# Performance work log

Hardware: AMD Instinct MI355X
Metric: run time of the kernel (lower is better)

## Reference

```python
import jax, jax.numpy as jnp
import numpy as np

DIM = 512      # model dim
HEADS = 8      # num heads
DH = 64        # dim_head (hard-coded in PerformerBlock)
M = 266        # nb_features = int(DH * ln(DH)) per performer_pytorch default
EPS = 1e-4     # softmax_kernel eps


def _gaussian_orthogonal_matrix(rng, m, d):
    # Faithful to performer_pytorch gaussian_orthogonal_random_matrix (scaling=0):
    # stacked QR-orthogonalized dxd blocks, rows rescaled by chi-distributed norms.
    blocks = []
    for _ in range(m // d + 1):
        q, _ = np.linalg.qr(rng.standard_normal((d, d)))
        blocks.append(q.T)
    mat = np.concatenate(blocks, 0)[:m]
    mult = np.linalg.norm(rng.standard_normal((m, d)), axis=1)
    return (mult[:, None] * mat).astype(np.float32)


def setup_inputs() -> dict:
    key = jax.random.key(0)
    ks = jax.random.split(key, 6)
    inner = HEADS * DH
    s = 0.02
    x = jax.random.normal(ks[0], (4, 4096, DIM), dtype=jnp.float32)
    Wq = jax.random.normal(ks[1], (inner, DIM), dtype=jnp.float32) * s
    Wk = jax.random.normal(ks[2], (inner, DIM), dtype=jnp.float32) * s
    Wv = jax.random.normal(ks[3], (inner, DIM), dtype=jnp.float32) * s
    Wo = jax.random.normal(ks[4], (DIM, inner), dtype=jnp.float32) * s
    bo = jnp.zeros((DIM,), dtype=jnp.float32)
    proj = jnp.asarray(_gaussian_orthogonal_matrix(np.random.default_rng(0), M, DH))
    return {"x": x, "Wq": Wq, "Wk": Wk, "Wv": Wv, "Wo": Wo, "bo": bo, "proj": proj}


def _softmax_kernel(t, proj, is_query):
    # t: (b,h,n,DH), proj: (M,DH)
    normalizer = DH ** -0.25          # 1/sqrt(sqrt(d))
    ratio = M ** -0.5
    td = jnp.einsum('bhnd,md->bhnm', t * normalizer, proj)
    diag = jnp.sum(t * t, axis=-1, keepdims=True) * 0.5 * (normalizer ** 2)
    if is_query:
        mx = jax.lax.stop_gradient(jnp.max(td, axis=-1, keepdims=True))
    else:
        mx = jax.lax.stop_gradient(jnp.max(td, axis=(-1, -2), keepdims=True))
    return ratio * (jnp.exp(td - diag - mx) + EPS)


def reference(x, Wq, Wk, Wv, Wo, bo, proj):
    b, n, _ = x.shape
    def heads(w):
        return jnp.einsum('bnd,ed->bne', x, w).reshape(b, n, HEADS, DH).transpose(0, 2, 1, 3)
    q, k, v = heads(Wq), heads(Wk), heads(Wv)  # (b,h,n,DH)
    qp = _softmax_kernel(q, proj, True)        # (b,h,n,M)
    kp = _softmax_kernel(k, proj, False)       # (b,h,n,M)
    # non-causal linear attention
    k_sum = jnp.sum(kp, axis=-2)                               # (b,h,M)
    d_inv = 1.0 / jnp.einsum('bhnm,bhm->bhn', qp, k_sum)       # (b,h,n)
    context = jnp.einsum('bhnm,bhnd->bhmd', kp, v)             # (b,h,M,DH)
    out = jnp.einsum('bhmd,bhnm,bhn->bhnd', context, qp, d_inv)
    out = out.transpose(0, 2, 1, 3).reshape(b, n, HEADS * DH)
    attn_out = out @ Wo.T + bo
    return x + attn_out
```

## Files before the change

### kernel.cpp

```cpp
#include <hip/hip_runtime.h>

#define N_ 4096
#define DIM_ 512
#define H_ 8
#define DH_ 64
#define M_ 266
#define MP_ 272
#define MP2_ 288
#define MP3_ 320
#define SLABM_ 280
#define NZ_ 8
#define NT_ 16384
#define BH_ 32

#define NORMC 0.3535533905932738f
#define RATIOC 0.06131393394849658f
#define EPSK 1e-4f
#define DIAGC 0.0625f
#define KA 0.51006971f
#define LOG2R -4.0276408f
#define LOG2E 1.4426950408889634f
#define REPS 6.131393e-6f

#define PROJP_B 0ul
#define KMAX_B  40960ul
#define KSUMA_B 41088ul
#define WO_B    82048ul
#define CTXT_B  606336ul
#define DIAGQ_B 1785984ul
#define DIAGK_B 2048128ul
#define XBF_B   2310272ul
#define WQ_B    19087488ul
#define WK_B    19611776ul
#define WV_B    20136064ul
#define CTXA_B  2310272ul
#define Q_B     20660352ul
#define K_B     37437568ul
#define VT_B    54214784ul
#define RMAXQ_B 70992000ul

typedef __bf16 bf16x8 __attribute__((ext_vector_type(8)));
typedef float f32x4 __attribute__((ext_vector_type(4)));
#define MFMA16(a, b, c) __builtin_amdgcn_mfma_f32_16x16x32_bf16((a), (b), (c), 0, 0, 0)

typedef __attribute__((address_space(1))) const unsigned int* gas_t;
typedef __attribute__((address_space(3))) unsigned int* las_t;
__device__ __forceinline__ void gload16(const void* g, void* l) {
  __builtin_amdgcn_global_load_lds((gas_t)g, (las_t)l, 16, 0, 0);
}

__device__ __forceinline__ float bfu(unsigned short u) {
  union { unsigned int i; float f; } x; x.i = ((unsigned int)u) << 16; return x.f;
}
__device__ __forceinline__ unsigned short f2bf(float f) {
  union { float f; unsigned int i; } u; u.f = f;
  unsigned int r = u.i + 0x7fffu + ((u.i >> 16) & 1u);
  return (unsigned short)(r >> 16);
}
__device__ __forceinline__ void atomicMaxF(float* addr, float val) {
  int* ai = (int*)addr;
  while (true) {
    float cur = __int_as_float(*(volatile int*)ai);
    if (val <= cur) break;
    int old = atomicCAS(ai, __float_as_int(cur), __float_as_int(val));
    if (old == __float_as_int(cur)) break;
  }
}

__global__ void cvt_kernel(const float* __restrict__ src, unsigned short* __restrict__ dst, int n) {
  int i = (blockIdx.x * 256 + threadIdx.x) * 4;
  const int stride = gridDim.x * 1024;
  for (; i < n; i += stride) {
    const float4 v = *(const float4*)(src + i);
    ushort4 u;
    u.x = f2bf(v.x); u.y = f2bf(v.y); u.z = f2bf(v.z); u.w = f2bf(v.w);
    *(ushort4*)(dst + i) = u;
  }
}

__global__ void setup_kernel(const float* __restrict__ proj,
                             unsigned short* __restrict__ projp,
                             float* __restrict__ kmax,
                             float* __restrict__ ksuma) {
  const int i = blockIdx.x * 256 + threadIdx.x;
  const int stride = gridDim.x * 256;
  for (int j = i; j < MP3_ * DH_; j += stride)
    projp[j] = (j < M_ * DH_) ? f2bf(proj[j]) : (unsigned short)0;
  for (int j = i; j < BH_; j += stride) kmax[j] = -3e38f;
  for (int j = i; j < BH_ * MP3_; j += stride) ksuma[j] = 0.f;
}

__global__ __launch_bounds__(256) void qkv_mfma(
    const unsigned short* __restrict__ x, const unsigned short* __restrict__ Wq,
    const unsigned short* __restrict__ Wk, const unsigned short* __restrict__ Wv,
    unsigned short* __restrict__ Q, unsigned short* __restrict__ K,
    unsigned short* __restrict__ VT) {
  __shared__ unsigned short As[128 * 64];
  __shared__ unsigned short Bs[128 * 64];
  const int z = blockIdx.z;
  const unsigned short* W = (z == 0) ? Wq : (z == 1) ? Wk : Wv;
  const int t0 = blockIdx.x * 128, e0 = blockIdx.y * 128;
  const int tid = threadIdx.x;
  const int wv = tid >> 6, lane = tid & 63;
  const int r = lane & 15, q = lane >> 4;
  const int wr = (wv >> 1) * 64, wc = (wv & 1) * 64;
  f32x4 acc[4][4];
#pragma unroll
  for (int i = 0; i < 4; ++i)
#pragma unroll
    for (int j = 0; j < 4; ++j) acc[i][j] = (f32x4){0.f, 0.f, 0.f, 0.f};
  const int lrow = lane >> 3, lcol = (lane & 7) * 8;
  for (int k0 = 0; k0 < DIM_; k0 += 64) {
#pragma unroll
    for (int j = 0; j < 4; ++j) {
      const int rr = wv * 32 + j * 8;
      gload16(&x[(size_t)(t0 + rr + lrow) * DIM_ + k0 + lcol], &As[rr * 64]);
      gload16(&W[(size_t)(e0 + rr + lrow) * DIM_ + k0 + lcol], &Bs[rr * 64]);
    }
    __syncthreads();
#pragma unroll
    for (int kc = 0; kc < 2; ++kc) {
      bf16x8 af[4], bfr[4];
#pragma unroll
      for (int rt = 0; rt < 4; ++rt)
        af[rt] = *(const bf16x8*)&As[(wr + rt * 16 + r) * 64 + kc * 32 + q * 8];
#pragma unroll
      for (int ct = 0; ct < 4; ++ct)
        bfr[ct] = *(const bf16x8*)&Bs[(wc + ct * 16 + r) * 64 + kc * 32 + q * 8];
#pragma unroll
      for (int rt = 0; rt < 4; ++rt)
#pragma unroll
        for (int ct = 0; ct < 4; ++ct)
          acc[rt][ct] = MFMA16(af[rt], bfr[ct], acc[rt][ct]);
    }
    __syncthreads();
  }
  if (z < 2) {
    unsigned short* dst = (z == 0) ? Q : K;
#pragma unroll
    for (int rt = 0; rt < 4; ++rt) {
#pragma unroll
      for (int ct = 0; ct < 4; ++ct) {
        const int e = e0 + wc + ct * 16 + r;
#pragma unroll
        for (int i = 0; i < 4; ++i) {
          const int t = t0 + wr + rt * 16 + q * 4 + i;
          dst[(size_t)t * DIM_ + e] = f2bf(acc[rt][ct][i]);
        }
      }
    }
  } else {
#pragma unroll
    for (int rt = 0; rt < 4; ++rt) {
      const int t = t0 + wr + rt * 16 + q * 4;
      const int b_ = t >> 12, n = t & (N_ - 1);
#pragma unroll
      for (int ct = 0; ct < 4; ++ct) {
        const int e = e0 + wc + ct * 16 + r;
        const int h = e >> 6, dh = e & 63;
        ushort4 pk;
        pk.x = f2bf(acc[rt][ct][0]); pk.y = f2bf(acc[rt][ct][1]);
        pk.z = f2bf(acc[rt][ct][2]); pk.w = f2bf(acc[rt][ct][3]);
        *(ushort4*)&VT[((size_t)((b_ * H_ + h) * DH_ + dh)) * N_ + n] = pk;
      }
    }
  }
}

__global__ void diag_kernel(const unsigned short* __restrict__ Q,
                            const unsigned short* __restrict__ K,
                            unsigned short* __restrict__ dq, unsigned short* __restrict__ dk) {
  const int i = blockIdx.x * 256 + threadIdx.x;
  const int bh = i >> 12, n = i & (N_ - 1);
  const int b_ = bh >> 3, h = bh & 7;
  const unsigned short* src = ((blockIdx.y == 0) ? Q : K) + (size_t)(b_ * N_ + n) * DIM_ + h * DH_;
  float s = 0.f;
#pragma unroll
  for (int c = 0; c < 16; ++c) {
    const ushort4 u = ((const ushort4*)src)[c];
    const float a = bfu(u.x), b2 = bfu(u.y), cc = bfu(u.z), d = bfu(u.w);
    s += a * a + b2 * b2 + cc * cc + d * d;
  }
  ((blockIdx.y == 0) ? dq : dk)[i] = f2bf(s * DIAGC);
}

__global__ __launch_bounds__(256) void kmax_mfma(
    const unsigned short* __restrict__ K, const unsigned short* __restrict__ Qb,
    const unsigned short* __restrict__ projp,
    float* __restrict__ kmax, float* __restrict__ rmaxq) {
  __shared__ unsigned short sP[MP_][72];
  __shared__ float wm[4];
  const int bh = blockIdx.x, n0 = blockIdx.y * 256;
  const int tid = threadIdx.x;
  const int wv = tid >> 6, lane = tid & 63;
  const int r = lane & 15, q = lane >> 4;
  const int b_ = bh >> 3, h = bh & 7;
  for (int c = tid; c < MP_ * 4; c += 256) {
    const int row = c >> 2, cb = (c & 3) * 8;
    *(uint4*)&sP[row][cb] = *(const uint4*)&projp[row * DH_ + cb];
  }
  bf16x8 kb[4][2], qb[4][2];
  const int nbase = n0 + wv * 64;
#pragma unroll
  for (int st = 0; st < 4; ++st) {
    const size_t off = (size_t)(b_ * N_ + nbase + st * 16 + r) * DIM_ + h * DH_;
    kb[st][0] = *(const bf16x8*)(K + off + q * 8);
    kb[st][1] = *(const bf16x8*)(K + off + 32 + q * 8);
    qb[st][0] = *(const bf16x8*)(Qb + off + q * 8);
    qb[st][1] = *(const bf16x8*)(Qb + off + 32 + q * 8);
  }
  __syncthreads();
  float km = -3e38f;
  float qm[4] = {-3e38f, -3e38f, -3e38f, -3e38f};
  for (int mt = 0; mt < 17; ++mt) {
    const bf16x8 p0 = *(const bf16x8*)&sP[mt * 16 + r][q * 8];
    const bf16x8 p1 = *(const bf16x8*)&sP[mt * 16 + r][32 + q * 8];
#pragma unroll
    for (int st = 0; st < 4; ++st) {
      f32x4 ka = (f32x4){0.f, 0.f, 0.f, 0.f};
      ka = MFMA16(p0, kb[st][0], ka);
      ka = MFMA16(p1, kb[st][1], ka);
      f32x4 qa = (f32x4){0.f, 0.f, 0.f, 0.f};
      qa = MFMA16(p0, qb[st][0], qa);
      qa = MFMA16(p1, qb[st][1], qa);
#pragma unroll
      for (int i = 0; i < 4; ++i) {
        const int m = mt * 16 + q * 4 + i;
        if (m < M_) {
          km = fmaxf(km, ka[i]);
          qm[st] = fmaxf(qm[st], qa[i]);
        }
      }
    }
  }
#pragma unroll
  for (int st = 0; st < 4; ++st) {
    float v = qm[st];
    v = fmaxf(v, __shfl_xor(v, 16, 64));
    v = fmaxf(v, __shfl_xor(v, 32, 64));
    if (q == 0) rmaxq[bh * N_ + nbase + st * 16 + r] = v;
  }
  for (int s2 = 1; s2 < 64; s2 <<= 1) km = fmaxf(km, __shfl_xor(km, s2, 64));
  if (lane == 0) wm[wv] = km;
  __syncthreads();
  if (tid == 0) {
    const float m = fmaxf(fmaxf(wm[0], wm[1]), fmaxf(wm[2], wm[3])) * NORMC;
    atomicMaxF(&kmax[bh], m);
  }
}

__global__ __launch_bounds__(256) void ctxfused_mfma(
    const unsigned short* __restrict__ K, const unsigned short* __restrict__ VT,
    const unsigned short* __restrict__ projp, const unsigned short* __restrict__ diag_k,
    const float* __restrict__ kmaxv, float* __restrict__ ksuma,
    float* __restrict__ slab) {
  __shared__ unsigned short kll[64][72];
  __shared__ unsigned short vtl[64][72];
  __shared__ unsigned short kpl[64][72];
  __shared__ float dgl[64];
  const int bh = blockIdx.x, m0 = blockIdx.y * 64, zi = blockIdx.z;
  const int nbase = zi * 512;
  const int tid = threadIdx.x;
  const int wv = tid >> 6, lane = tid & 63;
  const int r = lane & 15, q = lane >> 4;
  const int b_ = bh >> 3, h = bh & 7;
  const float km = kmaxv[bh];
  const unsigned short* prow = projp + (size_t)(m0 + wv * 16 + r) * DH_;
  const bf16x8 p0 = *(const bf16x8*)(prow + q * 8);
  const bf16x8 p1 = *(const bf16x8*)(prow + 32 + q * 8);
  const unsigned short* kbase = K + (size_t)(b_ * N_) * DIM_ + h * DH_;
  const unsigned short* vbase = VT + (size_t)bh * DH_ * N_;
  f32x4 cacc[4];
#pragma unroll
  for (int i = 0; i < 4; ++i) cacc[i] = (f32x4){0.f, 0.f, 0.f, 0.f};
  float ksa[4] = {0.f, 0.f, 0.f, 0.f};
  for (int nc = 0; nc < 8; ++nc) {
    const int n0c = nbase + nc * 64;
#pragma unroll
    for (int j = 0; j < 4; ++j) {
      const int idx = tid + j * 256;
      const int rr = idx >> 4, c4 = (idx & 15) << 2;
      *(ushort4*)&kll[rr][c4] = *(const ushort4*)&kbase[(size_t)(n0c + rr) * DIM_ + c4];
      *(ushort4*)&vtl[rr][c4] = *(const ushort4*)&vbase[(size_t)rr * N_ + n0c + c4];
    }
    if (tid < 16) {
      const ushort4 du = *(const ushort4*)&diag_k[bh * N_ + n0c + tid * 4];
      dgl[tid * 4 + 0] = bfu(du.x); dgl[tid * 4 + 1] = bfu(du.y);
      dgl[tid * 4 + 2] = bfu(du.z); dgl[tid * 4 + 3] = bfu(du.w);
    }
    __syncthreads();
#pragma unroll
    for (int nt = 0; nt < 4; ++nt) {
      const bf16x8 kb0 = *(const bf16x8*)&kll[nt * 16 + r][q * 8];
      const bf16x8 kb1 = *(const bf16x8*)&kll[nt * 16 + r][32 + q * 8];
      f32x4 acc = (f32x4){0.f, 0.f, 0.f, 0.f};
      acc = MFMA16(p0, kb0, acc);
      acc = MFMA16(p1, kb1, acc);
      const float dgk = dgl[nt * 16 + r];
#pragma unroll
      for (int i = 0; i < 4; ++i) {
        const int m = m0 + wv * 16 + q * 4 + i;
        float kp = 0.f;
        if (m < M_) {
          const float arg = fminf(NORMC * acc[i] - dgk - km, 0.f);
          kp = RATIOC * (__expf(arg) + EPSK);
        }
        kpl[wv * 16 + q * 4 + i][nt * 16 + r] = f2bf(kp);
        ksa[i] += kp;
      }
    }
    __syncthreads();
    {
      const bf16x8 a0 = *(const bf16x8*)&kpl[wv * 16 + r][q * 8];
      const bf16x8 a1 = *(const bf16x8*)&kpl[wv * 16 + r][32 + q * 8];
#pragma unroll
      for (int ct = 0; ct < 4; ++ct) {
        const bf16x8 b0 = *(const bf16x8*)&vtl[ct * 16 + r][q * 8];
        const bf16x8 b1 = *(const bf16x8*)&vtl[ct * 16 + r][32 + q * 8];
        cacc[ct] = MFMA16(a0, b0, cacc[ct]);
        cacc[ct] = MFMA16(a1, b1, cacc[ct]);
      }
    }
    __syncthreads();
  }
#pragma unroll
  for (int i = 0; i < 4; ++i)
    for (int s2 = 1; s2 < 16; s2 <<= 1) ksa[i] += __shfl_xor(ksa[i], s2, 64);
  if (r == 0) {
#pragma unroll
    for (int i = 0; i < 4; ++i)
      atomicAdd(&ksuma[bh * MP3_ + m0 + wv * 16 + q * 4 + i], ksa[i]);
  }
  float* sl = slab + (size_t)(bh * NZ_ + zi) * SLABM_ * DH_;
#pragma unroll
  for (int ct = 0; ct < 4; ++ct) {
#pragma unroll
    for (int i = 0; i < 4; ++i) {
      const int m = m0 + wv * 16 + q * 4 + i;
      if (m < SLABM_) sl[(size_t)m * DH_ + ct * 16 + r] = cacc[ct][i];
    }
  }
}

__global__ __launch_bounds__(256) void pack_kernel(const float* __restrict__ slab,
                                                   unsigned short* __restrict__ ctxT) {
  __shared__ float t[64][65];
  const int bh = blockIdx.x, m0 = blockIdx.y * 64;
  const int tid = threadIdx.x;
  const int mr = tid >> 4, d4 = (tid & 15) * 4;
#pragma unroll
  for (int pass = 0; pass < 4; ++pass) {
    const int ml = pass * 16 + mr;
    const int m = m0 + ml;
    float4 s = {0.f, 0.f, 0.f, 0.f};
    if (m < SLABM_) {
#pragma unroll
      for (int z = 0; z < NZ_; ++z) {
        const float4 v =
            *(const float4*)&slab[((size_t)(bh * NZ_ + z) * SLABM_ + m) * DH_ + d4];
        s.x += v.x; s.y += v.y; s.z += v.z; s.w += v.w;
      }
    }
    t[ml][d4 + 0] = s.x; t[ml][d4 + 1] = s.y; t[ml][d4 + 2] = s.z; t[ml][d4 + 3] = s.w;
  }
  __syncthreads();
  const int mc = tid & 63, dbase = tid >> 6;
  const int mo = m0 + mc;
  if (mo < MP2_) {
#pragma unroll
    for (int j = 0; j < 16; ++j) {
      const int d = dbase + j * 4;
      ctxT[((size_t)bh * DH_ + d) * MP2_ + mo] = f2bf(t[mc][d]);
    }
  }
}

__global__ __launch_bounds__(256) void qpout_mfma(
    const unsigned short* __restrict__ Qb, const unsigned short* __restrict__ projp,
    const float* __restrict__ rmaxq,
    const unsigned short* __restrict__ diag_q, const float* __restrict__ ksuma,
    const unsigned short* __restrict__ ctxT, unsigned short* __restrict__ attn) {
  __shared__ union SM {
    unsigned short sP[MP_][72];
    unsigned int qps[4][16][149];
  } sm;
  const int bh = blockIdx.x, n0 = blockIdx.y * 64;
  const int tid = threadIdx.x;
  const int wv = tid >> 6, lane = tid & 63;
  const int r = lane & 15, q = lane >> 4;
  const int b_ = bh >> 3, h = bh & 7;
  for (int c = tid; c < MP_ * 4; c += 256) {
    const int row = c >> 2, cb = (c & 3) * 8;
    *(uint4*)&sm.sP[row][cb] = *(const uint4*)&projp[row * DH_ + cb];
  }
  bf16x8 qb0, qb1;
  {
    const unsigned short* qrow = Qb + (size_t)(b_ * N_ + n0 + wv * 16 + r) * DIM_ + h * DH_;
    qb0 = *(const bf16x8*)(qrow + q * 8);
    qb1 = *(const bf16x8*)(qrow + 32 + q * 8);
  }
  const float rm = rmaxq[bh * N_ + n0 + wv * 16 + r];
  const float dg = bfu(diag_q[bh * N_ + n0 + wv * 16 + r]);
  const float Cl = LOG2R - dg * LOG2E - rm * KA;
  __syncthreads();
  unsigned int pk0[17], pk1[17];
  float part = 0.f;
#pragma unroll
  for (int mt = 0; mt < 17; ++mt) {
    const bf16x8 p0 = *(const bf16x8*)&sm.sP[mt * 16 + r][q * 8];
    const bf16x8 p1 = *(const bf16x8*)&sm.sP[mt * 16 + r][32 + q * 8];
    f32x4 acc = (f32x4){0.f, 0.f, 0.f, 0.f};
    acc = MFMA16(p0, qb0, acc);
    acc = MFMA16(p1, qb1, acc);
    const f32x4 kl = *(const f32x4*)&ksuma[bh * MP3_ + mt * 16 + q * 4];
    {
      const float s0 = fminf(acc[0] * KA + Cl, LOG2R);
      const float s1 = fminf(acc[1] * KA + Cl, LOG2R);
      const float e0 = exp2f(s0) + REPS;
      const float e1 = exp2f(s1) + REPS;
      unsigned int pkk;
      asm("v_cvt_pk_bf16_f32 %0, %1, %2" : "=v"(pkk) : "v"(e0), "v"(e1));
      pk0[mt] = pkk;
      union { unsigned int u; float f; } lo, hi;
      lo.u = pkk << 16; hi.u = pkk & 0xffff0000u;
      part += lo.f * kl[0] + hi.f * kl[1];
    }
    {
      const float s0 = fminf(acc[2] * KA + Cl, LOG2R);
      const float s1 = fminf(acc[3] * KA + Cl, LOG2R);
      const float e0 = exp2f(s0) + REPS;
      const float e1 = exp2f(s1) + REPS;
      unsigned int pkk;
      asm("v_cvt_pk_bf16_f32 %0, %1, %2" : "=v"(pkk) : "v"(e0), "v"(e1));
      pk1[mt] = pkk;
      union { unsigned int u; float f; } lo, hi;
      lo.u = pkk << 16; hi.u = pkk & 0xffff0000u;
      part += lo.f * kl[2] + hi.f * kl[3];
    }
  }
  __syncthreads();
#pragma unroll
  for (int mt = 0; mt < 17; ++mt)
    *(uint2*)&sm.qps[wv][r][mt * 8 + q * 2] = make_uint2(pk0[mt], pk1[mt]);
  *(uint2*)&sm.qps[wv][r][136 + q * 2] = make_uint2(0u, 0u);
  part += __shfl_xor(part, 16, 64);
  part += __shfl_xor(part, 32, 64);
  const float dinv = 1.f / fmaxf(part, 1e-30f);
  f32x4 oacc[4];
#pragma unroll
  for (int i = 0; i < 4; ++i) oacc[i] = (f32x4){0.f, 0.f, 0.f, 0.f};
  const unsigned short* cbase = ctxT + (size_t)bh * DH_ * MP2_;
#pragma unroll
  for (int kc = 0; kc < 9; ++kc) {
    const bf16x8 af = *(const bf16x8*)&sm.qps[wv][r][kc * 16 + q * 4];
#pragma unroll
    for (int dt = 0; dt < 4; ++dt) {
      const bf16x8 bfr = *(const bf16x8*)&cbase[(size_t)(dt * 16 + r) * MP2_ + kc * 32 + q * 8];
      oacc[dt] = MFMA16(af, bfr, oacc[dt]);
    }
  }
  float dv[4];
#pragma unroll
  for (int i = 0; i < 4; ++i)
    dv[i] = __shfl(dinv, (lane & 48) | (q * 4 + i), 64);
#pragma unroll
  for (int dt = 0; dt < 4; ++dt) {
    const int d = dt * 16 + r;
#pragma unroll
    for (int i = 0; i < 4; ++i) {
      const int nn = wv * 16 + q * 4 + i;
      attn[(size_t)(b_ * N_ + n0 + nn) * DIM_ + h * DH_ + d] = f2bf(oacc[dt][i] * dv[i]);
    }
  }
}

__global__ __launch_bounds__(256) void final_mfma(
    const unsigned short* __restrict__ attn, const unsigned short* __restrict__ Wo,
    const float* __restrict__ bo, const float* __restrict__ x,
    float* __restrict__ out) {
  __shared__ unsigned short As[128 * 64];
  __shared__ unsigned short Bs[128 * 64];
  const int t0 = blockIdx.x * 128, e0 = blockIdx.y * 128;
  const int tid = threadIdx.x;
  const int wv = tid >> 6, lane = tid & 63;
  const int r = lane & 15, q = lane >> 4;
  const int wr = (wv >> 1) * 64, wc = (wv & 1) * 64;
  f32x4 acc[4][4];
#pragma unroll
  for (int i = 0; i < 4; ++i)
#pragma unroll
    for (int j = 0; j < 4; ++j) acc[i][j] = (f32x4){0.f, 0.f, 0.f, 0.f};
  const int lrow = lane >> 3, lcol = (lane & 7) * 8;
  for (int k0 = 0; k0 < DIM_; k0 += 64) {
#pragma unroll
    for (int j = 0; j < 4; ++j) {
      const int rr = wv * 32 + j * 8;
      gload16(&attn[(size_t)(t0 + rr + lrow) * DIM_ + k0 + lcol], &As[rr * 64]);
      gload16(&Wo[(size_t)(e0 + rr + lrow) * DIM_ + k0 + lcol], &Bs[rr * 64]);
    }
    __syncthreads();
#pragma unroll
    for (int kc = 0; kc < 2; ++kc) {
      bf16x8 af[4], bfr[4];
#pragma unroll
      for (int rt = 0; rt < 4; ++rt)
        af[rt] = *(const bf16x8*)&As[(wr + rt * 16 + r) * 64 + kc * 32 + q * 8];
#pragma unroll
      for (int ct = 0; ct < 4; ++ct)
        bfr[ct] = *(const bf16x8*)&Bs[(wc + ct * 16 + r) * 64 + kc * 32 + q * 8];
#pragma unroll
      for (int rt = 0; rt < 4; ++rt)
#pragma unroll
        for (int ct = 0; ct < 4; ++ct)
          acc[rt][ct] = MFMA16(af[rt], bfr[ct], acc[rt][ct]);
    }
    __syncthreads();
  }
#pragma unroll
  for (int rt = 0; rt < 4; ++rt) {
#pragma unroll
    for (int ct = 0; ct < 4; ++ct) {
      const int c = e0 + wc + ct * 16 + r;
      const float bov = bo[c];
#pragma unroll
      for (int i = 0; i < 4; ++i) {
        const int t = t0 + wr + rt * 16 + q * 4 + i;
        out[(size_t)t * DIM_ + c] = acc[rt][ct][i] + bov + x[(size_t)t * DIM_ + c];
      }
    }
  }
}

extern "C" void kernel_launch(void* const* d_in, const int* in_sizes, int n_in,
                              void* d_out, int out_size, void* d_ws, size_t ws_size,
                              hipStream_t stream) {
  const float* x = (const float*)d_in[0];
  const float* Wq = (const float*)d_in[1];
  const float* Wk = (const float*)d_in[2];
  const float* Wv = (const float*)d_in[3];
  const float* Wo = (const float*)d_in[4];
  const float* bo = (const float*)d_in[5];
  const float* proj = (const float*)d_in[6];
  char* ws = (char*)d_ws;
  unsigned short* projp = (unsigned short*)(ws + PROJP_B);
  float* kmax = (float*)(ws + KMAX_B);
  float* ksuma = (float*)(ws + KSUMA_B);
  float* ctxa = (float*)(ws + CTXA_B);
  unsigned short* ctxT = (unsigned short*)(ws + CTXT_B);
  unsigned short* diag_q = (unsigned short*)(ws + DIAGQ_B);
  unsigned short* diag_k = (unsigned short*)(ws + DIAGK_B);
  unsigned short* xbf = (unsigned short*)(ws + XBF_B);
  unsigned short* wqb = (unsigned short*)(ws + WQ_B);
  unsigned short* wkb = (unsigned short*)(ws + WK_B);
  unsigned short* wvb = (unsigned short*)(ws + WV_B);
  unsigned short* wob = (unsigned short*)(ws + WO_B);
  unsigned short* Q = (unsigned short*)(ws + Q_B);
  unsigned short* K = (unsigned short*)(ws + K_B);
  unsigned short* VT = (unsigned short*)(ws + VT_B);
  float* rmaxq = (float*)(ws + RMAXQ_B);
  unsigned short* attn = K;
  float* out = (float*)d_out;

  cvt_kernel<<<1024, 256, 0, stream>>>(x, xbf, 8388608);
  cvt_kernel<<<128, 256, 0, stream>>>(Wq, wqb, 262144);
  cvt_kernel<<<128, 256, 0, stream>>>(Wk, wkb, 262144);
  cvt_kernel<<<128, 256, 0, stream>>>(Wv, wvb, 262144);
  cvt_kernel<<<128, 256, 0, stream>>>(Wo, wob, 262144);
  setup_kernel<<<80, 256, 0, stream>>>(proj, projp, kmax, ksuma);
  qkv_mfma<<<dim3(NT_ / 128, DIM_ / 128, 3), 256, 0, stream>>>(xbf, wqb, wkb, wvb, Q, K, VT);
  diag_kernel<<<dim3(512, 2), 256, 0, stream>>>(Q, K, diag_q, diag_k);
  kmax_mfma<<<dim3(BH_, N_ / 256), 256, 0, stream>>>(K, Q, projp, kmax, rmaxq);
  ctxfused_mfma<<<dim3(BH_, 5, NZ_), 256, 0, stream>>>(K, VT, projp, diag_k, kmax, ksuma, ctxa);
  pack_kernel<<<dim3(BH_, 5), 256, 0, stream>>>(ctxa, ctxT);
  qpout_mfma<<<dim3(BH_, 64), 256, 0, stream>>>(Q, projp, rmaxq, diag_q, ksuma, ctxT, attn);
  final_mfma<<<dim3(NT_ / 128, DIM_ / 128), 256, 0, stream>>>(attn, wob, bo, x, out);
}
```

Baseline: 292.6 us.

## Double-buffer LDS in projection GEMMs and merge prep kernels into one launch

Result: faster. 284.2 us (-2.9%).

```diff
diff --git a/kernel.cpp b/kernel.cpp
--- a/kernel.cpp
+++ b/kernel.cpp
@@ -67,27 +67,37 @@
   }
 }
 
-__global__ void cvt_kernel(const float* __restrict__ src, unsigned short* __restrict__ dst, int n) {
-  int i = (blockIdx.x * 256 + threadIdx.x) * 4;
-  const int stride = gridDim.x * 1024;
-  for (; i < n; i += stride) {
-    const float4 v = *(const float4*)(src + i);
+__global__ void prep_kernel(const float* __restrict__ x, const float* __restrict__ Wq,
+                            const float* __restrict__ Wk, const float* __restrict__ Wv,
+                            const float* __restrict__ Wo, const float* __restrict__ proj,
+                            unsigned short* __restrict__ xbf, unsigned short* __restrict__ wqb,
+                            unsigned short* __restrict__ wkb, unsigned short* __restrict__ wvb,
+                            unsigned short* __restrict__ wob,
+                            unsigned short* __restrict__ projp,
+                            float* __restrict__ kmax, float* __restrict__ ksuma) {
+  const int t0 = blockIdx.x * 256 + threadIdx.x;
+  const int stride = gridDim.x * 256;
+  for (int i = t0; i < 8388608 / 4; i += stride) {
+    const float4 v = ((const float4*)x)[i];
     ushort4 u;
     u.x = f2bf(v.x); u.y = f2bf(v.y); u.z = f2bf(v.z); u.w = f2bf(v.w);
-    *(ushort4*)(dst + i) = u;
-  }
-}
-
-__global__ void setup_kernel(const float* __restrict__ proj,
-                             unsigned short* __restrict__ projp,
-                             float* __restrict__ kmax,
-                             float* __restrict__ ksuma) {
-  const int i = blockIdx.x * 256 + threadIdx.x;
-  const int stride = gridDim.x * 256;
-  for (int j = i; j < MP3_ * DH_; j += stride)
+    ((ushort4*)xbf)[i] = u;
+  }
+  const float* wsrc[4] = {Wq, Wk, Wv, Wo};
+  unsigned short* wdst[4] = {wqb, wkb, wvb, wob};
+#pragma unroll
+  for (int w = 0; w < 4; ++w) {
+    for (int i = t0; i < 262144 / 4; i += stride) {
+      const float4 v = ((const float4*)wsrc[w])[i];
+      ushort4 u;
+      u.x = f2bf(v.x); u.y = f2bf(v.y); u.z = f2bf(v.z); u.w = f2bf(v.w);
+      ((ushort4*)wdst[w])[i] = u;
+    }
+  }
+  for (int j = t0; j < MP3_ * DH_; j += stride)
     projp[j] = (j < M_ * DH_) ? f2bf(proj[j]) : (unsigned short)0;
-  for (int j = i; j < BH_; j += stride) kmax[j] = -3e38f;
-  for (int j = i; j < BH_ * MP3_; j += stride) ksuma[j] = 0.f;
+  for (int j = t0; j < BH_; j += stride) kmax[j] = -3e38f;
+  for (int j = t0; j < BH_ * MP3_; j += stride) ksuma[j] = 0.f;
 }
 
 __global__ __launch_bounds__(256) void qkv_mfma(
@@ -95,8 +105,8 @@
     const unsigned short* __restrict__ Wk, const unsigned short* __restrict__ Wv,
     unsigned short* __restrict__ Q, unsigned short* __restrict__ K,
     unsigned short* __restrict__ VT) {
-  __shared__ unsigned short As[128 * 64];
-  __shared__ unsigned short Bs[128 * 64];
+  __shared__ unsigned short As[2][128 * 64];
+  __shared__ unsigned short Bs[2][128 * 64];
   const int z = blockIdx.z;
   const unsigned short* W = (z == 0) ? Wq : (z == 1) ? Wk : Wv;
   const int t0 = blockIdx.x * 128, e0 = blockIdx.y * 128;
@@ -110,31 +120,38 @@
 #pragma unroll
     for (int j = 0; j < 4; ++j) acc[i][j] = (f32x4){0.f, 0.f, 0.f, 0.f};
   const int lrow = lane >> 3, lcol = (lane & 7) * 8;
-  for (int k0 = 0; k0 < DIM_; k0 += 64) {
-#pragma unroll
-    for (int j = 0; j < 4; ++j) {
-      const int rr = wv * 32 + j * 8;
-      gload16(&x[(size_t)(t0 + rr + lrow) * DIM_ + k0 + lcol], &As[rr * 64]);
-      gload16(&W[(size_t)(e0 + rr + lrow) * DIM_ + k0 + lcol], &Bs[rr * 64]);
-    }
+#define QKV_STAGE(buf, k0)                                                          \
+  {                                                                                 \
+    _Pragma("unroll") for (int j = 0; j < 4; ++j) {                                 \
+      const int rr = wv * 32 + j * 8;                                               \
+      gload16(&x[(size_t)(t0 + rr + lrow) * DIM_ + (k0) + lcol], &As[buf][rr * 64]);\
+      gload16(&W[(size_t)(e0 + rr + lrow) * DIM_ + (k0) + lcol], &Bs[buf][rr * 64]);\
+    }                                                                               \
+  }
+#define QKV_COMPUTE(buf)                                                            \
+  {                                                                                 \
+    _Pragma("unroll") for (int kc = 0; kc < 2; ++kc) {                              \
+      bf16x8 af[4], bfr[4];                                                         \
+      _Pragma("unroll") for (int rt = 0; rt < 4; ++rt)                              \
+        af[rt] = *(const bf16x8*)&As[buf][(wr + rt * 16 + r) * 64 + kc * 32 + q * 8];\
+      _Pragma("unroll") for (int ct = 0; ct < 4; ++ct)                              \
+        bfr[ct] = *(const bf16x8*)&Bs[buf][(wc + ct * 16 + r) * 64 + kc * 32 + q * 8];\
+      _Pragma("unroll") for (int rt = 0; rt < 4; ++rt)                              \
+        _Pragma("unroll") for (int ct = 0; ct < 4; ++ct)                            \
+          acc[rt][ct] = MFMA16(af[rt], bfr[ct], acc[rt][ct]);                       \
+    }                                                                               \
+  }
+  QKV_STAGE(0, 0);
+  __syncthreads();
+  int cur = 0;
+#pragma unroll
+  for (int k0 = 64; k0 < DIM_; k0 += 64) {
+    QKV_STAGE(cur ^ 1, k0);
+    QKV_COMPUTE(cur);
     __syncthreads();
-#pragma unroll
-    for (int kc = 0; kc < 2; ++kc) {
-      bf16x8 af[4], bfr[4];
-#pragma unroll
-      for (int rt = 0; rt < 4; ++rt)
-        af[rt] = *(const bf16x8*)&As[(wr + rt * 16 + r) * 64 + kc * 32 + q * 8];
-#pragma unroll
-      for (int ct = 0; ct < 4; ++ct)
-        bfr[ct] = *(const bf16x8*)&Bs[(wc + ct * 16 + r) * 64 + kc * 32 + q * 8];
-#pragma unroll
-      for (int rt = 0; rt < 4; ++rt)
-#pragma unroll
-        for (int ct = 0; ct < 4; ++ct)
-          acc[rt][ct] = MFMA16(af[rt], bfr[ct], acc[rt][ct]);
-    }
-    __syncthreads();
-  }
+    cur ^= 1;
+  }
+  QKV_COMPUTE(cur);
   if (z < 2) {
     unsigned short* dst = (z == 0) ? Q : K;
 #pragma unroll
@@ -478,8 +495,8 @@
     const unsigned short* __restrict__ attn, const unsigned short* __restrict__ Wo,
     const float* __restrict__ bo, const float* __restrict__ x,
     float* __restrict__ out) {
-  __shared__ unsigned short As[128 * 64];
-  __shared__ unsigned short Bs[128 * 64];
+  __shared__ unsigned short As[2][128 * 64];
+  __shared__ unsigned short Bs[2][128 * 64];
   const int t0 = blockIdx.x * 128, e0 = blockIdx.y * 128;
   const int tid = threadIdx.x;
   const int wv = tid >> 6, lane = tid & 63;
@@ -491,31 +508,38 @@
 #pragma unroll
     for (int j = 0; j < 4; ++j) acc[i][j] = (f32x4){0.f, 0.f, 0.f, 0.f};
   const int lrow = lane >> 3, lcol = (lane & 7) * 8;
-  for (int k0 = 0; k0 < DIM_; k0 += 64) {
-#pragma unroll
-    for (int j = 0; j < 4; ++j) {
-      const int rr = wv * 32 + j * 8;
-      gload16(&attn[(size_t)(t0 + rr + lrow) * DIM_ + k0 + lcol], &As[rr * 64]);
-      gload16(&Wo[(size_t)(e0 + rr + lrow) * DIM_ + k0 + lcol], &Bs[rr * 64]);
-    }
+#define FIN_STAGE(buf, k0)                                                              \
+  {                                                                                     \
+    _Pragma("unroll") for (int j = 0; j < 4; ++j) {                                     \
+      const int rr = wv * 32 + j * 8;                                                   \
+      gload16(&attn[(size_t)(t0 + rr + lrow) * DIM_ + (k0) + lcol], &As[buf][rr * 64]); \
+      gload16(&Wo[(size_t)(e0 + rr + lrow) * DIM_ + (k0) + lcol], &Bs[buf][rr * 64]);   \
+    }                                                                                   \
+  }
+#define FIN_COMPUTE(buf)                                                                \
+  {                                                                                     \
+    _Pragma("unroll") for (int kc = 0; kc < 2; ++kc) {                                  \
+      bf16x8 af[4], bfr[4];                                                             \
+      _Pragma("unroll") for (int rt = 0; rt < 4; ++rt)                                  \
+        af[rt] = *(const bf16x8*)&As[buf][(wr + rt * 16 + r) * 64 + kc * 32 + q * 8];   \
+      _Pragma("unroll") for (int ct = 0; ct < 4; ++ct)                                  \
+        bfr[ct] = *(const bf16x8*)&Bs[buf][(wc + ct * 16 + r) * 64 + kc * 32 + q * 8];  \
+      _Pragma("unroll") for (int rt = 0; rt < 4; ++rt)                                  \
+        _Pragma("unroll") for (int ct = 0; ct < 4; ++ct)                                \
+          acc[rt][ct] = MFMA16(af[rt], bfr[ct], acc[rt][ct]);                           \
+    }                                                                                   \
+  }
+  FIN_STAGE(0, 0);
+  __syncthreads();
+  int cur = 0;
+#pragma unroll
+  for (int k0 = 64; k0 < DIM_; k0 += 64) {
+    FIN_STAGE(cur ^ 1, k0);
+    FIN_COMPUTE(cur);
     __syncthreads();
-#pragma unroll
-    for (int kc = 0; kc < 2; ++kc) {
-      bf16x8 af[4], bfr[4];
-#pragma unroll
-      for (int rt = 0; rt < 4; ++rt)
-        af[rt] = *(const bf16x8*)&As[(wr + rt * 16 + r) * 64 + kc * 32 + q * 8];
-#pragma unroll
-      for (int ct = 0; ct < 4; ++ct)
-        bfr[ct] = *(const bf16x8*)&Bs[(wc + ct * 16 + r) * 64 + kc * 32 + q * 8];
-#pragma unroll
-      for (int rt = 0; rt < 4; ++rt)
-#pragma unroll
-        for (int ct = 0; ct < 4; ++ct)
-          acc[rt][ct] = MFMA16(af[rt], bfr[ct], acc[rt][ct]);
-    }
-    __syncthreads();
-  }
+    cur ^= 1;
+  }
+  FIN_COMPUTE(cur);
 #pragma unroll
   for (int rt = 0; rt < 4; ++rt) {
 #pragma unroll
@@ -561,12 +585,8 @@
   unsigned short* attn = K;
   float* out = (float*)d_out;
 
-  cvt_kernel<<<1024, 256, 0, stream>>>(x, xbf, 8388608);
-  cvt_kernel<<<128, 256, 0, stream>>>(Wq, wqb, 262144);
-  cvt_kernel<<<128, 256, 0, stream>>>(Wk, wkb, 262144);
-  cvt_kernel<<<128, 256, 0, stream>>>(Wv, wvb, 262144);
-  cvt_kernel<<<128, 256, 0, stream>>>(Wo, wob, 262144);
-  setup_kernel<<<80, 256, 0, stream>>>(proj, projp, kmax, ksuma);
+  prep_kernel<<<1024, 256, 0, stream>>>(x, Wq, Wk, Wv, Wo, proj,
+                                        xbf, wqb, wkb, wvb, wob, projp, kmax, ksuma);
   qkv_mfma<<<dim3(NT_ / 128, DIM_ / 128, 3), 256, 0, stream>>>(xbf, wqb, wkb, wvb, Q, K, VT);
   diag_kernel<<<dim3(512, 2), 256, 0, stream>>>(Q, K, diag_q, diag_k);
   kmax_mfma<<<dim3(BH_, N_ / 256), 256, 0, stream>>>(K, Q, projp, kmax, rmaxq);
```

## Fuse conversion launches, fold diag into kmax, stage Q/K stores through LDS

Applied to the files above, without the earlier changes.

Result: faster. 275.3 us (-5.9%).

```diff
diff --git a/kernel.cpp b/kernel.cpp
--- a/kernel.cpp
+++ b/kernel.cpp
@@ -67,27 +67,37 @@
   }
 }
 
-__global__ void cvt_kernel(const float* __restrict__ src, unsigned short* __restrict__ dst, int n) {
-  int i = (blockIdx.x * 256 + threadIdx.x) * 4;
-  const int stride = gridDim.x * 1024;
-  for (; i < n; i += stride) {
-    const float4 v = *(const float4*)(src + i);
+__global__ void prep_kernel(const float* __restrict__ x, const float* __restrict__ Wq,
+                            const float* __restrict__ Wk, const float* __restrict__ Wv,
+                            const float* __restrict__ Wo, const float* __restrict__ proj,
+                            unsigned short* __restrict__ xbf, unsigned short* __restrict__ wqb,
+                            unsigned short* __restrict__ wkb, unsigned short* __restrict__ wvb,
+                            unsigned short* __restrict__ wob,
+                            unsigned short* __restrict__ projp,
+                            float* __restrict__ kmax, float* __restrict__ ksuma) {
+  const int t0 = blockIdx.x * 256 + threadIdx.x;
+  const int stride = gridDim.x * 256;
+  for (int i = t0; i < 8388608 / 4; i += stride) {
+    const float4 v = ((const float4*)x)[i];
     ushort4 u;
     u.x = f2bf(v.x); u.y = f2bf(v.y); u.z = f2bf(v.z); u.w = f2bf(v.w);
-    *(ushort4*)(dst + i) = u;
-  }
-}
-
-__global__ void setup_kernel(const float* __restrict__ proj,
-                             unsigned short* __restrict__ projp,
-                             float* __restrict__ kmax,
-                             float* __restrict__ ksuma) {
-  const int i = blockIdx.x * 256 + threadIdx.x;
-  const int stride = gridDim.x * 256;
-  for (int j = i; j < MP3_ * DH_; j += stride)
+    ((ushort4*)xbf)[i] = u;
+  }
+  const float* wsrc[4] = {Wq, Wk, Wv, Wo};
+  unsigned short* wdst[4] = {wqb, wkb, wvb, wob};
+#pragma unroll
+  for (int w = 0; w < 4; ++w) {
+    for (int i = t0; i < 262144 / 4; i += stride) {
+      const float4 v = ((const float4*)wsrc[w])[i];
+      ushort4 u;
+      u.x = f2bf(v.x); u.y = f2bf(v.y); u.z = f2bf(v.z); u.w = f2bf(v.w);
+      ((ushort4*)wdst[w])[i] = u;
+    }
+  }
+  for (int j = t0; j < MP3_ * DH_; j += stride)
     projp[j] = (j < M_ * DH_) ? f2bf(proj[j]) : (unsigned short)0;
-  for (int j = i; j < BH_; j += stride) kmax[j] = -3e38f;
-  for (int j = i; j < BH_ * MP3_; j += stride) ksuma[j] = 0.f;
+  for (int j = t0; j < BH_; j += stride) kmax[j] = -3e38f;
+  for (int j = t0; j < BH_ * MP3_; j += stride) ksuma[j] = 0.f;
 }
 
 __global__ __launch_bounds__(256) void qkv_mfma(
@@ -95,8 +105,9 @@
     const unsigned short* __restrict__ Wk, const unsigned short* __restrict__ Wv,
     unsigned short* __restrict__ Q, unsigned short* __restrict__ K,
     unsigned short* __restrict__ VT) {
-  __shared__ unsigned short As[128 * 64];
-  __shared__ unsigned short Bs[128 * 64];
+  __shared__ __align__(16) unsigned short S[128 * 136];
+  unsigned short* As = S;
+  unsigned short* Bs = S + 8192;
   const int z = blockIdx.z;
   const unsigned short* W = (z == 0) ? Wq : (z == 1) ? Wk : Wv;
   const int t0 = blockIdx.x * 128, e0 = blockIdx.y * 128;
@@ -138,17 +149,18 @@
   if (z < 2) {
     unsigned short* dst = (z == 0) ? Q : K;
 #pragma unroll
-    for (int rt = 0; rt < 4; ++rt) {
-#pragma unroll
-      for (int ct = 0; ct < 4; ++ct) {
-        const int e = e0 + wc + ct * 16 + r;
-#pragma unroll
-        for (int i = 0; i < 4; ++i) {
-          const int t = t0 + wr + rt * 16 + q * 4 + i;
-          dst[(size_t)t * DIM_ + e] = f2bf(acc[rt][ct][i]);
-        }
-      }
-    }
+    for (int rt = 0; rt < 4; ++rt)
+#pragma unroll
+      for (int ct = 0; ct < 4; ++ct)
+#pragma unroll
+        for (int i = 0; i < 4; ++i)
+          S[(wr + rt * 16 + q * 4 + i) * 136 + wc + ct * 16 + r] = f2bf(acc[rt][ct][i]);
+    __syncthreads();
+    const int row = tid >> 1, cb = (tid & 1) * 64;
+#pragma unroll
+    for (int j = 0; j < 8; ++j)
+      *(uint4*)&dst[(size_t)(t0 + row) * DIM_ + e0 + cb + j * 8] =
+          *(const uint4*)&S[row * 136 + cb + j * 8];
   } else {
 #pragma unroll
     for (int rt = 0; rt < 4; ++rt) {
@@ -167,27 +179,11 @@
   }
 }
 
-__global__ void diag_kernel(const unsigned short* __restrict__ Q,
-                            const unsigned short* __restrict__ K,
-                            unsigned short* __restrict__ dq, unsigned short* __restrict__ dk) {
-  const int i = blockIdx.x * 256 + threadIdx.x;
-  const int bh = i >> 12, n = i & (N_ - 1);
-  const int b_ = bh >> 3, h = bh & 7;
-  const unsigned short* src = ((blockIdx.y == 0) ? Q : K) + (size_t)(b_ * N_ + n) * DIM_ + h * DH_;
-  float s = 0.f;
-#pragma unroll
-  for (int c = 0; c < 16; ++c) {
-    const ushort4 u = ((const ushort4*)src)[c];
-    const float a = bfu(u.x), b2 = bfu(u.y), cc = bfu(u.z), d = bfu(u.w);
-    s += a * a + b2 * b2 + cc * cc + d * d;
-  }
-  ((blockIdx.y == 0) ? dq : dk)[i] = f2bf(s * DIAGC);
-}
-
 __global__ __launch_bounds__(256) void kmax_mfma(
     const unsigned short* __restrict__ K, const unsigned short* __restrict__ Qb,
     const unsigned short* __restrict__ projp,
-    float* __restrict__ kmax, float* __restrict__ rmaxq) {
+    float* __restrict__ kmax, float* __restrict__ rmaxq,
+    unsigned short* __restrict__ dq, unsigned short* __restrict__ dk) {
   __shared__ unsigned short sP[MP_][72];
   __shared__ float wm[4];
   const int bh = blockIdx.x, n0 = blockIdx.y * 256;
@@ -208,6 +204,25 @@
     kb[st][1] = *(const bf16x8*)(K + off + 32 + q * 8);
     qb[st][0] = *(const bf16x8*)(Qb + off + q * 8);
     qb[st][1] = *(const bf16x8*)(Qb + off + 32 + q * 8);
+  }
+#pragma unroll
+  for (int st = 0; st < 4; ++st) {
+    float sk = 0.f, sq = 0.f;
+#pragma unroll
+    for (int p = 0; p < 2; ++p)
+#pragma unroll
+      for (int e = 0; e < 8; ++e) {
+        const float kv = (float)kb[st][p][e];
+        const float qv = (float)qb[st][p][e];
+        sk += kv * kv;
+        sq += qv * qv;
+      }
+    sk += __shfl_xor(sk, 16, 64); sk += __shfl_xor(sk, 32, 64);
+    sq += __shfl_xor(sq, 16, 64); sq += __shfl_xor(sq, 32, 64);
+    if (q == 0) {
+      dk[bh * N_ + nbase + st * 16 + r] = f2bf(sk * DIAGC);
+      dq[bh * N_ + nbase + st * 16 + r] = f2bf(sq * DIAGC);
+    }
   }
   __syncthreads();
   float km = -3e38f;
@@ -561,15 +576,10 @@
   unsigned short* attn = K;
   float* out = (float*)d_out;
 
-  cvt_kernel<<<1024, 256, 0, stream>>>(x, xbf, 8388608);
-  cvt_kernel<<<128, 256, 0, stream>>>(Wq, wqb, 262144);
-  cvt_kernel<<<128, 256, 0, stream>>>(Wk, wkb, 262144);
-  cvt_kernel<<<128, 256, 0, stream>>>(Wv, wvb, 262144);
-  cvt_kernel<<<128, 256, 0, stream>>>(Wo, wob, 262144);
-  setup_kernel<<<80, 256, 0, stream>>>(proj, projp, kmax, ksuma);
+  prep_kernel<<<1024, 256, 0, stream>>>(x, Wq, Wk, Wv, Wo, proj,
+                                        xbf, wqb, wkb, wvb, wob, projp, kmax, ksuma);
   qkv_mfma<<<dim3(NT_ / 128, DIM_ / 128, 3), 256, 0, stream>>>(xbf, wqb, wkb, wvb, Q, K, VT);
-  diag_kernel<<<dim3(512, 2), 256, 0, stream>>>(Q, K, diag_q, diag_k);
-  kmax_mfma<<<dim3(BH_, N_ / 256), 256, 0, stream>>>(K, Q, projp, kmax, rmaxq);
+  kmax_mfma<<<dim3(BH_, N_ / 256), 256, 0, stream>>>(K, Q, projp, kmax, rmaxq, diag_q, diag_k);
   ctxfused_mfma<<<dim3(BH_, 5, NZ_), 256, 0, stream>>>(K, VT, projp, diag_k, kmax, ksuma, ctxa);
   pack_kernel<<<dim3(BH_, 5), 256, 0, stream>>>(ctxa, ctxT);
   qpout_mfma<<<dim3(BH_, 64), 256, 0, stream>>>(Q, projp, rmaxq, diag_q, ksuma, ctxT, attn);
```
